# Kernel tuning notes

Hardware: AMD Instinct MI355X
Metric: run time of the kernel (lower is better)

The kernel has to match this reference:

```python
import jax, jax.numpy as jnp
import numpy as np

B, A, N_IN = 128, 96, 128  # molecules, atoms per molecule, feature dim
H1, H2 = 64, 1             # gated-equivariant MLP widths: 128 -> 64 -> 1


def _mlp(x, W1, b1, W2, b2):
    return jax.nn.silu(x @ W1 + b1) @ W2 + b2


def _gated_block(s, v, Wmix, Ws1, bs1, Ws2, bs2, n_out, sact):
    # s: [N, n_sin], v: [N, 3, n_vin]
    vmix = jnp.einsum('ndi,io->ndo', v, Wmix)          # [N, 3, 2*n_out]
    vV, vW = vmix[..., :n_out], vmix[..., n_out:]
    vVn = jnp.linalg.norm(vV, axis=-2)                 # [N, n_out]
    x = _mlp(jnp.concatenate([s, vVn], axis=-1), Ws1, bs1, Ws2, bs2)
    s_out, gate = x[..., :n_out], x[..., n_out:]
    v_out = gate[:, None, :] * vW                      # [N, 3, n_out]
    if sact:
        s_out = jax.nn.silu(s_out)
    return s_out, v_out


def setup_inputs():
    key = jax.random.key(0)
    ks = iter(jax.random.split(key, 40))
    def W(shape):
        return jax.random.normal(next(ks), shape, jnp.float32) / np.sqrt(shape[0]).astype(np.float32)
    N = B * A
    return dict(
        positions=jax.random.normal(next(ks), (N, 3), jnp.float32) * 3.0,
        scalar_rep=jax.random.normal(next(ks), (N, N_IN), jnp.float32),
        vector_rep=jax.random.normal(next(ks), (N, 3, N_IN), jnp.float32),
        mix_W1=W((N_IN, 2 * H1)),
        sc1_W1=W((N_IN + H1, N_IN)), sc1_b1=jnp.zeros((N_IN,), jnp.float32),
        sc1_W2=W((N_IN, 2 * H1)), sc1_b2=jnp.zeros((2 * H1,), jnp.float32),
        mix_W2=W((H1, 2 * H2)),
        sc2_W1=W((H1 + H2, H1)), sc2_b1=jnp.zeros((H1,), jnp.float32),
        sc2_W2=W((H1, 2 * H2)), sc2_b2=jnp.zeros((2 * H2,), jnp.float32),
        vv_W1=W((9, 30)), vv_b1=jnp.zeros((30,), jnp.float32), vv_W2=W((30, 9)), vv_b2=jnp.zeros((9,), jnp.float32),
        vr_W1=W((9, 30)), vr_b1=jnp.zeros((30,), jnp.float32), vr_W2=W((30, 9)), vr_b2=jnp.zeros((9,), jnp.float32),
        s_W1=W((2, 30)), s_b1=jnp.zeros((30,), jnp.float32), s_W2=W((30, 9)), s_b2=jnp.zeros((9,), jnp.float32),
        h_W1=W((9, 30)), h_b1=jnp.zeros((30,), jnp.float32), h_W2=W((30, 9)), h_b2=jnp.zeros((9,), jnp.float32),
        n_atoms=jnp.full((B,), A, dtype=jnp.int32),
    )


def reference(positions, scalar_rep, vector_rep,
              mix_W1, sc1_W1, sc1_b1, sc1_W2, sc1_b2,
              mix_W2, sc2_W1, sc2_b1, sc2_W2, sc2_b2,
              vv_W1, vv_b1, vv_W2, vv_b2,
              vr_W1, vr_b1, vr_W2, vr_b2,
              s_W1, s_b1, s_W2, s_b2,
              h_W1, h_b1, h_W2, h_b2, n_atoms):
    # outnet: gated equivariant MLP 128 -> 64 (silu on scalars) -> 1 (no sact)
    s, v = _gated_block(scalar_rep, vector_rep, mix_W1, sc1_W1, sc1_b1, sc1_W2, sc1_b2, H1, True)
    s, v = _gated_block(s, v, mix_W2, sc2_W1, sc2_b1, sc2_W2, sc2_b2, H2, False)
    l0 = s[:, 0].reshape(B, A)          # [B, A]
    l1 = v[:, :, 0].reshape(B, A, 3)    # [B, A, 3]
    pos = positions.reshape(B, A, 3)
    # per-pair outer products, flattened 3x3 -> 9 (row-major k,l as in torch view)
    vv = jnp.einsum('bik,bjl->bijkl', l1, l1).reshape(B, A, A, 9)
    vr = jnp.einsum('bik,bjl->bijkl', l1, pos).reshape(B, A, A, 9)
    vv = _mlp(vv, vv_W1, vv_b1, vv_W2, vv_b2)
    vr = _mlp(vr, vr_W1, vr_b1, vr_W2, vr_b2)
    sp = jnp.stack([jnp.broadcast_to(l0[:, :, None], (B, A, A)),
                    jnp.broadcast_to(l0[:, None, :], (B, A, A))], axis=-1)  # [B,A,A,2] = (s_i, s_j)
    sp = _mlp(sp, s_W1, s_b1, s_W2, s_b2)
    h = _mlp(vv + vr + sp, h_W1, h_b1, h_W2, h_b2).reshape(B, A, A, 3, 3)
    # permute(0,2,1,3) per molecule -> block Hessian [3A, 3A]
    h = jnp.transpose(h, (0, 1, 3, 2, 4)).reshape(B, 3 * A, 3 * A)
    return h.reshape(-1, 27)
```

## Files before the change

kernel.cpp:

```cpp
#include <hip/hip_runtime.h>
#include <cstddef>

#define A_ATOMS 96
#define BATCH   128
#define NNODES  12288
#define NB      8
#define AS      132
#define XS      196
#define PSTR    240

typedef float v2f __attribute__((ext_vector_type(2)));

__device__ __forceinline__ float silu_f(float x) {
    float e = __expf(-x);
    return x * __builtin_amdgcn_rcpf(1.0f + e);
}
__device__ __forceinline__ v2f silu2(v2f x) {
    v2f r; r.x = silu_f(x.x); r.y = silu_f(x.y); return r;
}

#define RED64(v) { v += __shfl_xor(v, 1); v += __shfl_xor(v, 2); v += __shfl_xor(v, 4); \
                   v += __shfl_xor(v, 8); v += __shfl_xor(v, 16); v += __shfl_xor(v, 32); }
#define RED16(v) { v += __shfl_xor(v, 1); v += __shfl_xor(v, 2); v += __shfl_xor(v, 4); \
                   v += __shfl_xor(v, 8); }

__global__ __launch_bounds__(128, 3)
void node_k(const float* __restrict__ vrep, const float* __restrict__ mixW1,
            const float* __restrict__ srep,
            const float* __restrict__ sc1W1, const float* __restrict__ sc1b1,
            const float* __restrict__ sc1W2, const float* __restrict__ sc1b2,
            const float* __restrict__ mixW2,
            const float* __restrict__ sc2W1, const float* __restrict__ sc2b1,
            const float* __restrict__ sc2W2, const float* __restrict__ sc2b2,
            const float* __restrict__ pos,
            const float* __restrict__ vvW1, const float* __restrict__ vrW1,
            const float* __restrict__ sW1,  const float* __restrict__ sb1,
            float* __restrict__ l0v, float* __restrict__ l1v,
            float* __restrict__ P) {
    __shared__ float AsL[24 * AS];
    __shared__ float xinS[NB * XS];
    __shared__ float s1s[2][4][64];
    __shared__ float pwp[NB][6];
    __shared__ float gateS[NB], l0S[NB];

    const int t  = threadIdx.x;
    const int w  = t >> 6;
    const int ln = t & 63;
    const int cx = ln & 15;
    const int ry = ln >> 4;
    const int cb = w * 64 + cx * 4;
    const int row0  = blockIdx.x * 24;
    const int node0 = blockIdx.x * NB;

#pragma unroll
    for (int it = 0; it < 6; it++) {
        const int idx = it * 128 + t;
        const int r   = idx >> 5;
        const int c4  = (idx & 31) * 4;
        *(float4*)&AsL[r * AS + c4] = *(const float4*)(vrep + (size_t)(row0 + r) * 128 + c4);
    }
#pragma unroll
    for (int it = 0; it < 2; it++) {
        const int idx = it * 128 + t;
        const int a   = idx >> 5;
        const int c4  = (idx & 31) * 4;
        *(float4*)&xinS[a * XS + c4] = *(const float4*)(srep + (size_t)(node0 + a) * 128 + c4);
    }
    __syncthreads();

    float acc[2][3][4];
#pragma unroll
    for (int p = 0; p < 2; p++)
#pragma unroll
        for (int d = 0; d < 3; d++)
#pragma unroll
            for (int j = 0; j < 4; j++) acc[p][d][j] = 0.0f;

    for (int kc = 0; kc < 128; kc += 8) {
        float a[2][3][8];
#pragma unroll
        for (int p = 0; p < 2; p++)
#pragma unroll
            for (int d = 0; d < 3; d++) {
                const int row = (3 * (ry + 4 * p) + d) * AS + kc;
                *(float4*)&a[p][d][0] = *(const float4*)&AsL[row];
                *(float4*)&a[p][d][4] = *(const float4*)&AsL[row + 4];
            }
#pragma unroll
        for (int kk = 0; kk < 8; kk++) {
            float b[4];
            *(float4*)b = *(const float4*)(mixW1 + (size_t)(kc + kk) * 128 + cb);
#pragma unroll
            for (int p = 0; p < 2; p++)
#pragma unroll
                for (int d = 0; d < 3; d++)
#pragma unroll
                    for (int j = 0; j < 4; j++)
                        acc[p][d][j] += a[p][d][kk] * b[j];
        }
    }
    if (w == 0) {
#pragma unroll
        for (int p = 0; p < 2; p++) {
            float nrm[4];
#pragma unroll
            for (int c = 0; c < 4; c++)
                nrm[c] = sqrtf(acc[p][0][c] * acc[p][0][c] + acc[p][1][c] * acc[p][1][c]
                             + acc[p][2][c] * acc[p][2][c]);
            *(float4*)&xinS[(ry + 4 * p) * XS + 128 + cb] = *(float4*)nrm;
        }
    }
    __syncthreads();

    float* workS = AsL;
    {
        float acc3[2][4];
#pragma unroll
        for (int p = 0; p < 2; p++)
#pragma unroll
            for (int j = 0; j < 4; j++) acc3[p][j] = 0.0f;
        for (int kc = 0; kc < 192; kc += 8) {
            float af[2][8];
#pragma unroll
            for (int p = 0; p < 2; p++) {
                const int row = (ry + 4 * p) * XS + kc;
                *(float4*)&af[p][0] = *(const float4*)&xinS[row];
                *(float4*)&af[p][4] = *(const float4*)&xinS[row + 4];
            }
#pragma unroll
            for (int kk = 0; kk < 8; kk++) {
                float b[4];
                *(float4*)b = *(const float4*)(sc1W1 + (size_t)(kc + kk) * 128 + cb);
#pragma unroll
                for (int p = 0; p < 2; p++)
#pragma unroll
                    for (int j = 0; j < 4; j++) acc3[p][j] += af[p][kk] * b[j];
            }
        }
#pragma unroll
        for (int p = 0; p < 2; p++) {
            float h[4];
#pragma unroll
            for (int j = 0; j < 4; j++) h[j] = silu_f(acc3[p][j] + sc1b1[cb + j]);
            *(float4*)&workS[(ry + 4 * p) * AS + cb] = *(float4*)h;
        }
    }
    __syncthreads();

    float xg[2][4];
    {
        float acc4[2][4];
#pragma unroll
        for (int p = 0; p < 2; p++)
#pragma unroll
            for (int j = 0; j < 4; j++) acc4[p][j] = 0.0f;
        for (int kc = 0; kc < 128; kc += 8) {
            float af[2][8];
#pragma unroll
            for (int p = 0; p < 2; p++) {
                const int row = (ry + 4 * p) * AS + kc;
                *(float4*)&af[p][0] = *(const float4*)&workS[row];
                *(float4*)&af[p][4] = *(const float4*)&workS[row + 4];
            }
#pragma unroll
            for (int kk = 0; kk < 8; kk++) {
                float b[4];
                *(float4*)b = *(const float4*)(sc1W2 + (size_t)(kc + kk) * 128 + cb);
#pragma unroll
                for (int p = 0; p < 2; p++)
#pragma unroll
                    for (int j = 0; j < 4; j++) acc4[p][j] += af[p][kk] * b[j];
            }
        }
        if (w == 0) {
#pragma unroll
            for (int p = 0; p < 2; p++) {
                float xs[4];
#pragma unroll
                for (int j = 0; j < 4; j++) xs[j] = acc4[p][j] + sc1b2[cb + j];
                *(float4*)&xinS[(ry + 4 * p) * XS + cb] = *(float4*)xs;
            }
        } else {
#pragma unroll
            for (int p = 0; p < 2; p++)
#pragma unroll
                for (int j = 0; j < 4; j++) xg[p][j] = acc4[p][j] + sc1b2[cb + j];
        }
    }

    if (w == 1) {
#pragma unroll
        for (int p = 0; p < 2; p++) {
            float p0 = 0, p1 = 0, p2 = 0, p3 = 0, p4 = 0, p5 = 0;
#pragma unroll
            for (int c = 0; c < 4; c++) {
                float2 m = *(const float2*)(mixW2 + (size_t)(cb - 64 + c) * 2);
                const float v0 = xg[p][c] * acc[p][0][c];
                const float v1 = xg[p][c] * acc[p][1][c];
                const float v2 = xg[p][c] * acc[p][2][c];
                p0 += v0 * m.x; p1 += v0 * m.y;
                p2 += v1 * m.x; p3 += v1 * m.y;
                p4 += v2 * m.x; p5 += v2 * m.y;
            }
            RED16(p0); RED16(p1); RED16(p2); RED16(p3); RED16(p4); RED16(p5);
            if (cx == 0) {
                const int nl = ry + 4 * p;
                pwp[nl][0] = p0; pwp[nl][1] = p1;
                pwp[nl][2] = p2; pwp[nl][3] = p3;
                pwp[nl][4] = p4; pwp[nl][5] = p5;
            }
        }
    }
    __syncthreads();

    {
        const float bb1 = sc2b1[ln];
        const float wn  = sc2W1[64 * 64 + ln];
        const float wq0 = sc2W2[ln * 2 + 0], wq1 = sc2W2[ln * 2 + 1];
        float vn2[4], g0[4], g1[4], g2[4];
#pragma unroll
        for (int r = 0; r < 4; r++) {
            const int nl = r * 2 + w;
            const float q00 = pwp[nl][0], q10 = pwp[nl][2], q20 = pwp[nl][4];
            vn2[r] = sqrtf(q00 * q00 + q10 * q10 + q20 * q20);
            g0[r] = pwp[nl][1]; g1[r] = pwp[nl][3]; g2[r] = pwp[nl][5];
            s1s[w][r][ln] = silu_f(xinS[nl * XS + ln]);
        }
        __builtin_amdgcn_s_waitcnt(0);
        float acc5[4];
#pragma unroll
        for (int r = 0; r < 4; r++) acc5[r] = bb1 + vn2[r] * wn;
#pragma unroll 8
        for (int i2 = 0; i2 < 64; i2++) {
            const float wv = sc2W1[i2 * 64 + ln];
#pragma unroll
            for (int r = 0; r < 4; r++) acc5[r] += s1s[w][r][i2] * wv;
        }
#pragma unroll
        for (int r = 0; r < 4; r++) {
            const float h2 = silu_f(acc5[r]);
            float q0 = h2 * wq0, q1 = h2 * wq1;
            RED64(q0); RED64(q1);
            if (ln == 0) {
                const int nl = r * 2 + w;
                const int n = node0 + nl;
                const float gate = q1 + sc2b2[1];
                const float l0o  = q0 + sc2b2[0];
                l0v[n] = l0o;
                l1v[(size_t)n * 3 + 0] = gate * g0[r];
                l1v[(size_t)n * 3 + 1] = gate * g1[r];
                l1v[(size_t)n * 3 + 2] = gate * g2[r];
                gateS[nl] = gate;
                l0S[nl]   = l0o;
            }
        }
    }
    __syncthreads();

    {
        const int nl = t >> 4;
        const int q  = t & 15;
        const int n  = node0 + nl;
        const float lj0 = gateS[nl] * pwp[nl][1];
        const float lj1 = gateS[nl] * pwp[nl][3];
        const float lj2 = gateS[nl] * pwp[nl][5];
        const float l0j = l0S[nl];
        const float pj0 = pos[n * 3 + 0], pj1 = pos[n * 3 + 1], pj2 = pos[n * 3 + 2];
        float* Pj = P + (size_t)n * PSTR;
        for (int h = q; h < 30; h += 16) {
            float o[8];
#pragma unroll
            for (int a = 0; a < 3; a++) {
                o[a]     = lj0 * vvW1[(3 * a + 0) * 30 + h]
                         + lj1 * vvW1[(3 * a + 1) * 30 + h]
                         + lj2 * vvW1[(3 * a + 2) * 30 + h];
                o[3 + a] = pj0 * vrW1[(3 * a + 0) * 30 + h]
                         + pj1 * vrW1[(3 * a + 1) * 30 + h]
                         + pj2 * vrW1[(3 * a + 2) * 30 + h];
            }
            o[6] = sb1[h] + l0j * sW1[30 + h];
            o[7] = 0.0f;
            *(float4*)&Pj[h * 8 + 0] = *(float4*)&o[0];
            *(float4*)&Pj[h * 8 + 4] = *(float4*)&o[4];
        }
    }
}

__global__ __launch_bounds__(192)
void pair_k(const float* __restrict__ l0v, const float* __restrict__ l1v,
            const float* __restrict__ P,
            const float* __restrict__ vvb1, const float* __restrict__ vrb1,
            const float* __restrict__ sW1,
            const float* __restrict__ vvW2, const float* __restrict__ vrW2,
            const float* __restrict__ sW2,
            const float* __restrict__ vvb2, const float* __restrict__ vrb2,
            const float* __restrict__ sb2,
            const float* __restrict__ hW1,  const float* __restrict__ hb1,
            const float* __restrict__ hW2,  const float* __restrict__ hb2,
            float* __restrict__ out) {
    const int t = threadIdx.x;
    const int b = blockIdx.y;
    const int g = (t >= 96) ? 1 : 0;
    const int j = t - g * 96;
    const int i0 = blockIdx.x * 8 + g * 4;
    const int ni0 = b * A_ATOMS + i0;
    const int ni2 = ni0 + 2;
    const int nj  = b * A_ATOMS + j;
    const float* Pj = P + (size_t)nj * PSTR;

    const v2f liA0 = { l1v[ni0 * 3 + 0], l1v[(ni0 + 1) * 3 + 0] };
    const v2f liA1 = { l1v[ni0 * 3 + 1], l1v[(ni0 + 1) * 3 + 1] };
    const v2f liA2 = { l1v[ni0 * 3 + 2], l1v[(ni0 + 1) * 3 + 2] };
    const v2f s0iA = { l0v[ni0], l0v[ni0 + 1] };
    const v2f liB0 = { l1v[ni2 * 3 + 0], l1v[(ni2 + 1) * 3 + 0] };
    const v2f liB1 = { l1v[ni2 * 3 + 1], l1v[(ni2 + 1) * 3 + 1] };
    const v2f liB2 = { l1v[ni2 * 3 + 2], l1v[(ni2 + 1) * 3 + 2] };
    const v2f s0iB = { l0v[ni2], l0v[ni2 + 1] };

    v2f tA[9], tB[9];
#pragma unroll
    for (int l = 0; l < 9; l++) {
        const float t0 = vvb2[l] + vrb2[l] + sb2[l];
        tA[l] = (v2f)t0; tB[l] = (v2f)t0;
    }

#pragma unroll 2
    for (int h = 0; h < 30; h++) {
        const float4 w0 = *(const float4*)&Pj[h * 8 + 0];
        const float4 w1 = *(const float4*)&Pj[h * 8 + 4];
        const float pv0 = w0.x, pv1 = w0.y, pv2 = w0.z;
        const float pr0 = w0.w, pr1 = w1.x, pr2 = w1.y;
        const float ps  = w1.z;
        const float sw  = sW1[h];
        const float bv = vvb1[h], br = vrb1[h];

        v2f avA = (v2f)(bv) + liA0 * pv0 + liA1 * pv1 + liA2 * pv2;
        v2f arA = (v2f)(br) + liA0 * pr0 + liA1 * pr1 + liA2 * pr2;
        v2f asA = (v2f)(ps) + s0iA * sw;
        v2f avB = (v2f)(bv) + liB0 * pv0 + liB1 * pv1 + liB2 * pv2;
        v2f arB = (v2f)(br) + liB0 * pr0 + liB1 * pr1 + liB2 * pr2;
        v2f asB = (v2f)(ps) + s0iB * sw;
        avA = silu2(avA); arA = silu2(arA); asA = silu2(asA);
        avB = silu2(avB); arB = silu2(arB); asB = silu2(asB);
#pragma unroll
        for (int l = 0; l < 9; l++) {
            const float w2v = vvW2[h * 9 + l];
            const float w2r = vrW2[h * 9 + l];
            const float w2s = sW2[h * 9 + l];
            tA[l] += avA * w2v + arA * w2r + asA * w2s;
            tB[l] += avB * w2v + arB * w2r + asB * w2s;
        }
    }

    v2f oA[9], oB[9];
#pragma unroll
    for (int l = 0; l < 9; l++) {
        oA[l] = (v2f)(hb2[l]); oB[l] = (v2f)(hb2[l]);
    }
#pragma unroll 2
    for (int h = 0; h < 30; h++) {
        v2f aA = (v2f)(hb1[h]), aB = (v2f)(hb1[h]);
#pragma unroll
        for (int m = 0; m < 9; m++) {
            const float w1 = hW1[m * 30 + h];
            aA += tA[m] * w1; aB += tB[m] * w1;
        }
        aA = silu2(aA); aB = silu2(aB);
#pragma unroll
        for (int l = 0; l < 9; l++) {
            const float w2 = hW2[h * 9 + l];
            oA[l] += aA * w2; oB[l] += aB * w2;
        }
    }

#pragma unroll
    for (int k = 0; k < 3; k++) {
        const size_t offA0 = ((size_t)ni0 * 3 + k) * 288 + (size_t)j * 3;
        const size_t offA1 = offA0 + 3 * 288;
        out[offA0 + 0] = oA[3 * k + 0].x;
        out[offA0 + 1] = oA[3 * k + 1].x;
        out[offA0 + 2] = oA[3 * k + 2].x;
        out[offA1 + 0] = oA[3 * k + 0].y;
        out[offA1 + 1] = oA[3 * k + 1].y;
        out[offA1 + 2] = oA[3 * k + 2].y;
        const size_t offB0 = ((size_t)ni2 * 3 + k) * 288 + (size_t)j * 3;
        const size_t offB1 = offB0 + 3 * 288;
        out[offB0 + 0] = oB[3 * k + 0].x;
        out[offB0 + 1] = oB[3 * k + 1].x;
        out[offB0 + 2] = oB[3 * k + 2].x;
        out[offB1 + 0] = oB[3 * k + 0].y;
        out[offB1 + 1] = oB[3 * k + 1].y;
        out[offB1 + 2] = oB[3 * k + 2].y;
    }
}

extern "C" void kernel_launch(void* const* d_in, const int* in_sizes, int n_in,
                              void* d_out, int out_size, void* d_ws, size_t ws_size,
                              hipStream_t stream) {
    const float* pos   = (const float*)d_in[0];
    const float* srep  = (const float*)d_in[1];
    const float* vrep  = (const float*)d_in[2];
    const float* mixW1 = (const float*)d_in[3];
    const float* sc1W1 = (const float*)d_in[4];
    const float* sc1b1 = (const float*)d_in[5];
    const float* sc1W2 = (const float*)d_in[6];
    const float* sc1b2 = (const float*)d_in[7];
    const float* mixW2 = (const float*)d_in[8];
    const float* sc2W1 = (const float*)d_in[9];
    const float* sc2b1 = (const float*)d_in[10];
    const float* sc2W2 = (const float*)d_in[11];
    const float* sc2b2 = (const float*)d_in[12];
    const float* vvW1  = (const float*)d_in[13];
    const float* vvb1  = (const float*)d_in[14];
    const float* vvW2  = (const float*)d_in[15];
    const float* vvb2  = (const float*)d_in[16];
    const float* vrW1  = (const float*)d_in[17];
    const float* vrb1  = (const float*)d_in[18];
    const float* vrW2  = (const float*)d_in[19];
    const float* vrb2  = (const float*)d_in[20];
    const float* sW1   = (const float*)d_in[21];
    const float* sb1   = (const float*)d_in[22];
    const float* sW2   = (const float*)d_in[23];
    const float* sb2   = (const float*)d_in[24];
    const float* hW1   = (const float*)d_in[25];
    const float* hb1   = (const float*)d_in[26];
    const float* hW2   = (const float*)d_in[27];
    const float* hb2   = (const float*)d_in[28];

    float* ws  = (float*)d_ws;
    float* P   = ws;
    float* l0v = P + (size_t)PSTR * NNODES;
    float* l1v = l0v + NNODES;
    float* outf = (float*)d_out;

    node_k<<<NNODES / NB, 128, 0, stream>>>(
        vrep, mixW1, srep,
        sc1W1, sc1b1, sc1W2, sc1b2,
        mixW2, sc2W1, sc2b1, sc2W2, sc2b2,
        pos, vvW1, vrW1, sW1, sb1,
        l0v, l1v, P);

    pair_k<<<dim3(A_ATOMS / 8, BATCH), 192, 0, stream>>>(
        l0v, l1v, P,
        vvb1, vrb1, sW1,
        vvW2, vrW2, sW2,
        vvb2, vrb2, sb2,
        hW1, hb1, hW2, hb2,
        outf);
}
```

Before: 261.8 us.

## Vectorize pair MLP over output features with inline v_pk_fma using SGPR weight pairs

Each thread in the pair kernel now handles 2 i-atoms instead of 4, and the grid doubles in x. Packing now runs over output-feature pairs, using inline-asm v_pk_fma_f32 with pairs of weights held in scalar registers and op_sel to broadcast a lane, rather than packing over atom pairs. The goal is fewer VGPRs and more occupancy, plus scalar-register weight operands. The cost is that each block reloads the P row per j twice as often, and the inline asm limits how the compiler can schedule.

```diff
diff --git a/kernel.cpp b/kernel.cpp
--- a/kernel.cpp
+++ b/kernel.cpp
@@ -10,13 +10,26 @@
 #define PSTR    240
 
 typedef float v2f __attribute__((ext_vector_type(2)));
+typedef unsigned long long u64;
 
 __device__ __forceinline__ float silu_f(float x) {
     float e = __expf(-x);
     return x * __builtin_amdgcn_rcpf(1.0f + e);
 }
-__device__ __forceinline__ v2f silu2(v2f x) {
-    v2f r; r.x = silu_f(x.x); r.y = silu_f(x.y); return r;
+
+__device__ __forceinline__ void pkfma(v2f& acc, v2f a, u64 w) {
+    asm("v_pk_fma_f32 %0, %1, %2, %0" : "+v"(acc) : "v"(a), "s"(w));
+}
+__device__ __forceinline__ void pkfma_lo(v2f& acc, v2f a, u64 w) {
+    asm("v_pk_fma_f32 %0, %1, %2, %0 op_sel:[0,0,0] op_sel_hi:[0,1,1]"
+        : "+v"(acc) : "v"(a), "s"(w));
+}
+__device__ __forceinline__ void pkfma_hi(v2f& acc, v2f a, u64 w) {
+    asm("v_pk_fma_f32 %0, %1, %2, %0 op_sel:[1,0,0] op_sel_hi:[1,1,1]"
+        : "+v"(acc) : "v"(a), "s"(w));
+}
+__device__ __forceinline__ u64 ldw2(const float* p) {
+    u64 w; __builtin_memcpy(&w, p, 8); return w;
 }
 
 #define RED64(v) { v += __shfl_xor(v, 1); v += __shfl_xor(v, 2); v += __shfl_xor(v, 4); \
@@ -302,95 +315,116 @@
     const int b = blockIdx.y;
     const int g = (t >= 96) ? 1 : 0;
     const int j = t - g * 96;
-    const int i0 = blockIdx.x * 8 + g * 4;
+    const int i0 = blockIdx.x * 4 + g * 2;
     const int ni0 = b * A_ATOMS + i0;
-    const int ni2 = ni0 + 2;
     const int nj  = b * A_ATOMS + j;
     const float* Pj = P + (size_t)nj * PSTR;
 
-    const v2f liA0 = { l1v[ni0 * 3 + 0], l1v[(ni0 + 1) * 3 + 0] };
-    const v2f liA1 = { l1v[ni0 * 3 + 1], l1v[(ni0 + 1) * 3 + 1] };
-    const v2f liA2 = { l1v[ni0 * 3 + 2], l1v[(ni0 + 1) * 3 + 2] };
-    const v2f s0iA = { l0v[ni0], l0v[ni0 + 1] };
-    const v2f liB0 = { l1v[ni2 * 3 + 0], l1v[(ni2 + 1) * 3 + 0] };
-    const v2f liB1 = { l1v[ni2 * 3 + 1], l1v[(ni2 + 1) * 3 + 1] };
-    const v2f liB2 = { l1v[ni2 * 3 + 2], l1v[(ni2 + 1) * 3 + 2] };
-    const v2f s0iB = { l0v[ni2], l0v[ni2 + 1] };
-
-    v2f tA[9], tB[9];
-#pragma unroll
-    for (int l = 0; l < 9; l++) {
-        const float t0 = vvb2[l] + vrb2[l] + sb2[l];
-        tA[l] = (v2f)t0; tB[l] = (v2f)t0;
-    }
+    const float li0x = l1v[ni0 * 3 + 0], li0y = l1v[ni0 * 3 + 1], li0z = l1v[ni0 * 3 + 2];
+    const float li1x = l1v[(ni0 + 1) * 3 + 0], li1y = l1v[(ni0 + 1) * 3 + 1],
+                li1z = l1v[(ni0 + 1) * 3 + 2];
+    const float s00 = l0v[ni0], s01 = l0v[ni0 + 1];
+
+    v2f tA0[4], tA1[4];
+    float t80, t81;
+#pragma unroll
+    for (int lp = 0; lp < 4; lp++) {
+        v2f tb = { vvb2[2 * lp] + vrb2[2 * lp] + sb2[2 * lp],
+                   vvb2[2 * lp + 1] + vrb2[2 * lp + 1] + sb2[2 * lp + 1] };
+        tA0[lp] = tb; tA1[lp] = tb;
+    }
+    t80 = t81 = vvb2[8] + vrb2[8] + sb2[8];
 
 #pragma unroll 2
     for (int h = 0; h < 30; h++) {
         const float4 w0 = *(const float4*)&Pj[h * 8 + 0];
         const float4 w1 = *(const float4*)&Pj[h * 8 + 4];
-        const float pv0 = w0.x, pv1 = w0.y, pv2 = w0.z;
-        const float pr0 = w0.w, pr1 = w1.x, pr2 = w1.y;
-        const float ps  = w1.z;
-        const float sw  = sW1[h];
-        const float bv = vvb1[h], br = vrb1[h];
-
-        v2f avA = (v2f)(bv) + liA0 * pv0 + liA1 * pv1 + liA2 * pv2;
-        v2f arA = (v2f)(br) + liA0 * pr0 + liA1 * pr1 + liA2 * pr2;
-        v2f asA = (v2f)(ps) + s0iA * sw;
-        v2f avB = (v2f)(bv) + liB0 * pv0 + liB1 * pv1 + liB2 * pv2;
-        v2f arB = (v2f)(br) + liB0 * pr0 + liB1 * pr1 + liB2 * pr2;
-        v2f asB = (v2f)(ps) + s0iB * sw;
-        avA = silu2(avA); arA = silu2(arA); asA = silu2(asA);
-        avB = silu2(avB); arB = silu2(arB); asB = silu2(asB);
-#pragma unroll
-        for (int l = 0; l < 9; l++) {
-            const float w2v = vvW2[h * 9 + l];
-            const float w2r = vrW2[h * 9 + l];
-            const float w2s = sW2[h * 9 + l];
-            tA[l] += avA * w2v + arA * w2r + asA * w2s;
-            tB[l] += avB * w2v + arB * w2r + asB * w2s;
-        }
-    }
-
-    v2f oA[9], oB[9];
-#pragma unroll
-    for (int l = 0; l < 9; l++) {
-        oA[l] = (v2f)(hb2[l]); oB[l] = (v2f)(hb2[l]);
-    }
-#pragma unroll 2
-    for (int h = 0; h < 30; h++) {
-        v2f aA = (v2f)(hb1[h]), aB = (v2f)(hb1[h]);
-#pragma unroll
-        for (int m = 0; m < 9; m++) {
-            const float w1 = hW1[m * 30 + h];
-            aA += tA[m] * w1; aB += tB[m] * w1;
-        }
-        aA = silu2(aA); aB = silu2(aB);
-#pragma unroll
-        for (int l = 0; l < 9; l++) {
-            const float w2 = hW2[h * 9 + l];
-            oA[l] += aA * w2; oB[l] += aB * w2;
-        }
-    }
-
+        const float bv = vvb1[h], br = vrb1[h], sw = sW1[h];
+        const u64 wv0 = ldw2(vvW2 + h * 9 + 0), wv1 = ldw2(vvW2 + h * 9 + 2);
+        const u64 wv2 = ldw2(vvW2 + h * 9 + 4), wv3 = ldw2(vvW2 + h * 9 + 6);
+        const u64 wr0 = ldw2(vrW2 + h * 9 + 0), wr1 = ldw2(vrW2 + h * 9 + 2);
+        const u64 wr2 = ldw2(vrW2 + h * 9 + 4), wr3 = ldw2(vrW2 + h * 9 + 6);
+        const u64 ws0 = ldw2(sW2 + h * 9 + 0),  ws1 = ldw2(sW2 + h * 9 + 2);
+        const u64 ws2 = ldw2(sW2 + h * 9 + 4),  ws3 = ldw2(sW2 + h * 9 + 6);
+        const float wv8 = vvW2[h * 9 + 8], wr8 = vrW2[h * 9 + 8], ws8 = sW2[h * 9 + 8];
+
+        const float av0 = silu_f(w0.x * li0x + w0.y * li0y + w0.z * li0z + bv);
+        const float ar0 = silu_f(w0.w * li0x + w1.x * li0y + w1.y * li0z + br);
+        const float as0 = silu_f(w1.z + s00 * sw);
+        const float av1 = silu_f(w0.x * li1x + w0.y * li1y + w0.z * li1z + bv);
+        const float ar1 = silu_f(w0.w * li1x + w1.x * li1y + w1.y * li1z + br);
+        const float as1 = silu_f(w1.z + s01 * sw);
+        const v2f avp = { av0, av1 }, arp = { ar0, ar1 }, asp = { as0, as1 };
+
+        pkfma_lo(tA0[0], avp, wv0); pkfma_lo(tA0[0], arp, wr0); pkfma_lo(tA0[0], asp, ws0);
+        pkfma_lo(tA0[1], avp, wv1); pkfma_lo(tA0[1], arp, wr1); pkfma_lo(tA0[1], asp, ws1);
+        pkfma_lo(tA0[2], avp, wv2); pkfma_lo(tA0[2], arp, wr2); pkfma_lo(tA0[2], asp, ws2);
+        pkfma_lo(tA0[3], avp, wv3); pkfma_lo(tA0[3], arp, wr3); pkfma_lo(tA0[3], asp, ws3);
+        pkfma_hi(tA1[0], avp, wv0); pkfma_hi(tA1[0], arp, wr0); pkfma_hi(tA1[0], asp, ws0);
+        pkfma_hi(tA1[1], avp, wv1); pkfma_hi(tA1[1], arp, wr1); pkfma_hi(tA1[1], asp, ws1);
+        pkfma_hi(tA1[2], avp, wv2); pkfma_hi(tA1[2], arp, wr2); pkfma_hi(tA1[2], asp, ws2);
+        pkfma_hi(tA1[3], avp, wv3); pkfma_hi(tA1[3], arp, wr3); pkfma_hi(tA1[3], asp, ws3);
+        t80 += av0 * wv8 + ar0 * wr8 + as0 * ws8;
+        t81 += av1 * wv8 + ar1 * wr8 + as1 * ws8;
+    }
+
+    v2f oA0[4], oA1[4];
+    float o80, o81;
+#pragma unroll
+    for (int lp = 0; lp < 4; lp++) {
+        v2f ob = { hb2[2 * lp], hb2[2 * lp + 1] };
+        oA0[lp] = ob; oA1[lp] = ob;
+    }
+    o80 = o81 = hb2[8];
+
+    const v2f t8p0 = { t80, t80 }, t8p1 = { t81, t81 };
+
+#pragma unroll 3
+    for (int hp = 0; hp < 15; hp++) {
+        const int h0 = 2 * hp, h1 = 2 * hp + 1;
+        v2f a0 = { hb1[h0], hb1[h1] };
+        v2f a1 = a0;
+#pragma unroll
+        for (int lp = 0; lp < 4; lp++) {
+            const u64 wm0 = ldw2(hW1 + (2 * lp) * 30 + h0);
+            const u64 wm1 = ldw2(hW1 + (2 * lp + 1) * 30 + h0);
+            pkfma_lo(a0, tA0[lp], wm0); pkfma_hi(a0, tA0[lp], wm1);
+            pkfma_lo(a1, tA1[lp], wm0); pkfma_hi(a1, tA1[lp], wm1);
+        }
+        const u64 w8 = ldw2(hW1 + 8 * 30 + h0);
+        pkfma(a0, t8p0, w8);
+        pkfma(a1, t8p1, w8);
+
+        const float sx0 = silu_f(a0.x), sy0 = silu_f(a0.y);
+        const float sx1 = silu_f(a1.x), sy1 = silu_f(a1.y);
+        const v2f sp0 = { sx0, sy0 }, sp1 = { sx1, sy1 };
+
+#pragma unroll
+        for (int lp = 0; lp < 4; lp++) {
+            const u64 u0 = ldw2(hW2 + h0 * 9 + 2 * lp);
+            const u64 u1 = ldw2(hW2 + h1 * 9 + 2 * lp);
+            pkfma_lo(oA0[lp], sp0, u0); pkfma_hi(oA0[lp], sp0, u1);
+            pkfma_lo(oA1[lp], sp1, u0); pkfma_hi(oA1[lp], sp1, u1);
+        }
+        const float z0 = hW2[h0 * 9 + 8], z1 = hW2[h1 * 9 + 8];
+        o80 += sx0 * z0 + sy0 * z1;
+        o81 += sx1 * z0 + sy1 * z1;
+    }
+
+    float q0[9] = { oA0[0].x, oA0[0].y, oA0[1].x, oA0[1].y,
+                    oA0[2].x, oA0[2].y, oA0[3].x, oA0[3].y, o80 };
+    float q1[9] = { oA1[0].x, oA1[0].y, oA1[1].x, oA1[1].y,
+                    oA1[2].x, oA1[2].y, oA1[3].x, oA1[3].y, o81 };
 #pragma unroll
     for (int k = 0; k < 3; k++) {
-        const size_t offA0 = ((size_t)ni0 * 3 + k) * 288 + (size_t)j * 3;
-        const size_t offA1 = offA0 + 3 * 288;
-        out[offA0 + 0] = oA[3 * k + 0].x;
-        out[offA0 + 1] = oA[3 * k + 1].x;
-        out[offA0 + 2] = oA[3 * k + 2].x;
-        out[offA1 + 0] = oA[3 * k + 0].y;
-        out[offA1 + 1] = oA[3 * k + 1].y;
-        out[offA1 + 2] = oA[3 * k + 2].y;
-        const size_t offB0 = ((size_t)ni2 * 3 + k) * 288 + (size_t)j * 3;
-        const size_t offB1 = offB0 + 3 * 288;
-        out[offB0 + 0] = oB[3 * k + 0].x;
-        out[offB0 + 1] = oB[3 * k + 1].x;
-        out[offB0 + 2] = oB[3 * k + 2].x;
-        out[offB1 + 0] = oB[3 * k + 0].y;
-        out[offB1 + 1] = oB[3 * k + 1].y;
-        out[offB1 + 2] = oB[3 * k + 2].y;
+        const size_t base0 = ((size_t)ni0 * 3 + k) * 288 + (size_t)j * 3;
+        out[base0 + 0] = q0[3 * k + 0];
+        out[base0 + 1] = q0[3 * k + 1];
+        out[base0 + 2] = q0[3 * k + 2];
+        const size_t base1 = base0 + 3 * 288;
+        out[base1 + 0] = q1[3 * k + 0];
+        out[base1 + 1] = q1[3 * k + 1];
+        out[base1 + 2] = q1[3 * k + 2];
     }
 }
 
@@ -440,7 +474,7 @@
         pos, vvW1, vrW1, sW1, sb1,
         l0v, l1v, P);
 
-    pair_k<<<dim3(A_ATOMS / 8, BATCH), 192, 0, stream>>>(
+    pair_k<<<dim3(A_ATOMS / 4, BATCH), 192, 0, stream>>>(
         l0v, l1v, P,
         vvb1, vrb1, sW1,
         vvW2, vrW2, sW2,
```

New measurement: 255.6 us, median of 2. 2.4% less time.
